# Optimization experiments

Measured on AMD Instinct MI355X. Metric: run time of the kernel, lower is better.

## Reference

```python
import jax, jax.numpy as jnp
import numpy as np

N_NODES = 20000
N_EDGES = 320000
IN_FEATS = 64
HIDDENS = [128, 128, 128]
K = 4        # n_kernels
DIM = 2      # pseudo_coord


def setup_inputs() -> dict:
    key = jax.random.key(0)
    ks = jax.random.split(key, 32)
    inp = {
        "features": jax.random.normal(ks[0], (N_NODES, IN_FEATS), dtype=jnp.float32),
        "pseudo": jax.random.uniform(ks[1], (N_EDGES, DIM), dtype=jnp.float32),
        "src": jax.random.randint(ks[2], (N_EDGES,), 0, N_NODES, dtype=jnp.int32),
        "dst": jax.random.randint(ks[3], (N_EDGES,), 0, N_NODES, dtype=jnp.int32),
    }
    dims_in = [IN_FEATS] + HIDDENS[:-1]
    ki = 4
    for i, (din, dout) in enumerate(zip(dims_in, HIDDENS)):
        inp[f"fc_w{i}"] = jax.random.normal(ks[ki], (din, K * dout), dtype=jnp.float32) * (1.0 / np.sqrt(din)); ki += 1
        inp[f"mu{i}"] = jax.random.normal(ks[ki], (K, DIM), dtype=jnp.float32) * 0.1; ki += 1
        inp[f"inv_sigma{i}"] = jnp.ones((K, DIM), dtype=jnp.float32)
        inp[f"bias{i}"] = jnp.zeros((dout,), dtype=jnp.float32)
        inp[f"pw{i}"] = jax.random.normal(ks[ki], (DIM, DIM), dtype=jnp.float32) * 0.5; ki += 1
        inp[f"pb{i}"] = jnp.zeros((DIM,), dtype=jnp.float32)
    return inp


def _gmm_layer(h, pseudo, src, dst, fc_w, mu, inv_sigma, bias, pw, pb):
    k, dim = mu.shape
    dout = fc_w.shape[1] // k
    hp = (h @ fc_w).reshape(-1, k, dout)              # [N, K, out]
    u = jnp.tanh(pseudo @ pw + pb)                    # [E, dim] per-layer pseudo projection
    diff = (u[:, None, :] - mu[None, :, :]) * inv_sigma[None, :, :]
    w = jnp.exp(-0.5 * jnp.sum(diff * diff, axis=-1))  # [E, K] Gaussian mixture weights
    msg = jnp.einsum('ek,eko->eo', w, hp[src])         # gather + weighted mix -> [E, out]
    agg = jax.ops.segment_sum(msg, dst, num_segments=h.shape[0])  # scatter-sum
    return agg + bias


def reference(features, pseudo, src, dst,
              fc_w0, mu0, inv_sigma0, bias0, pw0, pb0,
              fc_w1, mu1, inv_sigma1, bias1, pw1, pb1,
              fc_w2, mu2, inv_sigma2, bias2, pw2, pb2):
    h = features
    h = _gmm_layer(h, pseudo, src, dst, fc_w0, mu0, inv_sigma0, bias0, pw0, pb0)
    h = _gmm_layer(h, pseudo, src, dst, fc_w1, mu1, inv_sigma1, bias1, pw1, pb1)
    h = _gmm_layer(h, pseudo, src, dst, fc_w2, mu2, inv_sigma2, bias2, pw2, pb2)
    return h
```

## Files before the change

kernel.cpp:

```cpp
#include <hip/hip_runtime.h>
#include <hip/hip_bf16.h>
#include <hip/hip_fp16.h>
#include <math.h>

#define NN 20000
#define NE 320000

typedef __attribute__((ext_vector_type(8))) short bf16x8;
typedef __attribute__((ext_vector_type(4))) float f32x4;

__device__ inline float bf2f_lo(uint v) {
    union { uint i; float f; } c; c.i = v << 16; return c.f;
}
__device__ inline float bf2f_hi(uint v) {
    union { uint i; float f; } c; c.i = v & 0xffff0000u; return c.f;
}
__device__ inline ushort f2bf(float f) {
    __hip_bfloat16 h = __float2bfloat16(f);
    return *reinterpret_cast<ushort*>(&h);
}
__device__ inline float2 h2f2(uint u) {
    union { uint i; __half2 h; } c; c.i = u;
    return __half22float2(c.h);
}
__device__ inline ushort f2h(float f) {
    __half h = __float2half_rn(f);
    return *reinterpret_cast<ushort*>(&h);
}

__global__ void count_kernel(const int* __restrict__ dst, int* __restrict__ counts) {
    int e = blockIdx.x * blockDim.x + threadIdx.x;
    if (e < NE) atomicAdd(&counts[dst[e]], 1);
}

__global__ __launch_bounds__(1024) void scan_kernel(const int* __restrict__ counts,
                                                    int* __restrict__ offsets,
                                                    int* __restrict__ cursor) {
    __shared__ int part[1024];
    const int T = 1024, CHK = (NN + T - 1) / T;
    int t = threadIdx.x;
    int begin = t * CHK;
    int c[CHK];
    int s = 0;
    bool full = (begin + CHK <= NN);
    if (full) {
#pragma unroll
        for (int q = 0; q < CHK / 4; ++q) {
            int4 v = *(const int4*)(counts + begin + q * 4);
            c[q * 4 + 0] = v.x; c[q * 4 + 1] = v.y; c[q * 4 + 2] = v.z; c[q * 4 + 3] = v.w;
        }
#pragma unroll
        for (int q = 0; q < CHK; ++q) s += c[q];
    } else {
        int end = begin + CHK < NN ? begin + CHK : NN;
        if (begin > NN) begin = NN;
        for (int i = begin; i < end; ++i) {
            int v = counts[i];
            c[i - begin] = v;
            s += v;
        }
    }
    part[t] = s;
    __syncthreads();
    for (int off = 1; off < T; off <<= 1) {
        int v = (t >= off) ? part[t - off] : 0;
        __syncthreads();
        part[t] += v;
        __syncthreads();
    }
    int run = (t == 0) ? 0 : part[t - 1];
    if (full) {
#pragma unroll
        for (int q = 0; q < CHK / 4; ++q) {
            int4 o;
            o.x = run; run += c[q * 4 + 0];
            o.y = run; run += c[q * 4 + 1];
            o.z = run; run += c[q * 4 + 2];
            o.w = run; run += c[q * 4 + 3];
            *(int4*)(offsets + begin + q * 4) = o;
            *(int4*)(cursor + begin + q * 4) = o;
        }
    } else {
        int end = begin + CHK < NN ? begin + CHK : NN;
        for (int i = begin; i < end; ++i) {
            offsets[i] = run;
            cursor[i] = run;
            run += c[i - begin];
        }
    }
    if (t == T - 1) offsets[NN] = part[T - 1];
}

__global__ void fill1_kernel(const int* __restrict__ dst, int* __restrict__ cursor,
                             int* __restrict__ csr_eidx) {
    int e = blockIdx.x * blockDim.x + threadIdx.x;
    if (e >= NE) return;
    int pos = atomicAdd(&cursor[dst[e]], 1);
    csr_eidx[pos] = e;
}

struct EdgeParams {
    const float *pw0, *pb0, *mu0, *is0;
    const float *pw1, *pb1, *mu1, *is1;
    const float *pw2, *pb2, *mu2, *is2;
};

__device__ inline float fast_tanh(float x) {
    x = fminf(fmaxf(x, -9.f), 9.f);
    float e = __expf(2.f * x);
    return 1.f - 2.f / (e + 1.f);
}

__device__ inline void layer_w(float p0, float p1, const float* pw, const float* pb,
                               const float* mu, const float* is, float* out4) {
    float u0 = fast_tanh(p0 * pw[0] + p1 * pw[2] + pb[0]);
    float u1 = fast_tanh(p0 * pw[1] + p1 * pw[3] + pb[1]);
#pragma unroll
    for (int k = 0; k < 4; ++k) {
        float d0 = (u0 - mu[k * 2 + 0]) * is[k * 2 + 0];
        float d1 = (u1 - mu[k * 2 + 1]) * is[k * 2 + 1];
        out4[k] = __expf(-0.5f * (d0 * d0 + d1 * d1));
    }
}

__global__ void fill2_prep(const int* __restrict__ csr_eidx, const int* __restrict__ src,
                           const float* __restrict__ pseudo, EdgeParams P,
                           int* __restrict__ csr_src, ushort* __restrict__ csr_w,
                           const float* __restrict__ f0, const float* __restrict__ f1,
                           const float* __restrict__ f2, ushort* __restrict__ w0,
                           ushort* __restrict__ w1, ushort* __restrict__ w2) {
    int bid = blockIdx.x;
    if (bid < 1250) {
        int i = bid * 256 + threadIdx.x;
        int e = csr_eidx[i];
        float2 p = *(const float2*)(pseudo + (size_t)e * 2);
        csr_src[i] = src[e];
        float w[4];
        uint2 pk;
        layer_w(p.x, p.y, P.pw0, P.pb0, P.mu0, P.is0, w);
        pk.x = (uint)f2h(w[0]) | ((uint)f2h(w[1]) << 16);
        pk.y = (uint)f2h(w[2]) | ((uint)f2h(w[3]) << 16);
        *(uint2*)(csr_w + (size_t)(0 * NE + i) * 4) = pk;
        layer_w(p.x, p.y, P.pw1, P.pb1, P.mu1, P.is1, w);
        pk.x = (uint)f2h(w[0]) | ((uint)f2h(w[1]) << 16);
        pk.y = (uint)f2h(w[2]) | ((uint)f2h(w[3]) << 16);
        *(uint2*)(csr_w + (size_t)(1 * NE + i) * 4) = pk;
        layer_w(p.x, p.y, P.pw2, P.pb2, P.mu2, P.is2, w);
        pk.x = (uint)f2h(w[0]) | ((uint)f2h(w[1]) << 16);
        pk.y = (uint)f2h(w[2]) | ((uint)f2h(w[3]) << 16);
        *(uint2*)(csr_w + (size_t)(2 * NE + i) * 4) = pk;
    } else {
        int idx = (bid - 1250) * 256 + threadIdx.x;
        const float* srcp;
        ushort* dstp;
        int din, KD, li;
        if (idx < 128 * 256) {
            srcp = f0; dstp = w0; din = 64; KD = 256; li = idx;
        } else if (idx < 128 * 256 + 128 * 512) {
            srcp = f1; dstp = w1; din = 128; KD = 512; li = idx - 128 * 256;
        } else {
            srcp = f2; dstp = w2; din = 128; KD = 512; li = idx - 128 * 256 - 128 * 512;
        }
        int n = li / KD;
        int r = li - n * KD;
        int k = r / din;
        int d = r - k * din;
        dstp[li] = f2bf(srcp[d * 512 + k * 128 + n]);
    }
}

template <int DIN, bool INF32, bool OUTBF>
__global__ __launch_bounds__(256, 4) void layer_fused(const void* __restrict__ hin,
                                                      const int* __restrict__ offsets,
                                                      const int* __restrict__ csr_src,
                                                      const ushort* __restrict__ csr_w,
                                                      const ushort* __restrict__ Bt,
                                                      const float* __restrict__ bias,
                                                      void* __restrict__ hout) {
    constexpr int KD = 4 * DIN;
    constexpr int PITCH = KD + 8;
    constexpr int BATCH = 16;
    __shared__ __align__(16) ushort Ts[16 * PITCH];
    int wv = threadIdx.x >> 6, lane = threadIdx.x & 63;
    int l16 = lane & 15, quad = lane >> 4;
    int nb = blockIdx.x * 16;

#pragma unroll
    for (int j = 0; j < 4; ++j) {
        int row = wv * 4 + j;
        int n = nb + row;
        int b = __builtin_amdgcn_readfirstlane(offsets[n]);
        int e = __builtin_amdgcn_readfirstlane(offsets[n + 1]);
        if (INF32) {
            const float* h = (const float*)hin;
            float a0 = 0.f, a1 = 0.f, a2 = 0.f, a3 = 0.f;
            for (int i = b; i < e; i += BATCH) {
                int s[BATCH]; uint wlo[BATCH], whi[BATCH]; float hv[BATCH];
#pragma unroll
                for (int u = 0; u < BATCH; ++u) {
                    int ii = i + u;
                    bool ok = ii < e;
                    int idx = ok ? ii : b;
                    s[u] = csr_src[idx];
                    uint2 wp = *(const uint2*)(csr_w + (size_t)idx * 4);
                    wlo[u] = ok ? wp.x : 0u;
                    whi[u] = ok ? wp.y : 0u;
                }
#pragma unroll
                for (int u = 0; u < BATCH; ++u) hv[u] = h[(size_t)s[u] * 64 + lane];
#pragma unroll
                for (int u = 0; u < BATCH; ++u) {
                    float2 wa = h2f2(wlo[u]);
                    float2 wb = h2f2(whi[u]);
                    a0 += wa.x * hv[u];
                    a1 += wa.y * hv[u];
                    a2 += wb.x * hv[u];
                    a3 += wb.y * hv[u];
                }
            }
            Ts[row * PITCH + 0 * 64 + lane] = f2bf(a0);
            Ts[row * PITCH + 1 * 64 + lane] = f2bf(a1);
            Ts[row * PITCH + 2 * 64 + lane] = f2bf(a2);
            Ts[row * PITCH + 3 * 64 + lane] = f2bf(a3);
        } else {
            const ushort* h = (const ushort*)hin;
            float a00 = 0.f, a01 = 0.f, a10 = 0.f, a11 = 0.f;
            float a20 = 0.f, a21 = 0.f, a30 = 0.f, a31 = 0.f;
            for (int i = b; i < e; i += BATCH) {
                int s[BATCH]; uint wlo[BATCH], whi[BATCH]; uint v[BATCH];
#pragma unroll
                for (int u = 0; u < BATCH; ++u) {
                    int ii = i + u;
                    bool ok = ii < e;
                    int idx = ok ? ii : b;
                    s[u] = csr_src[idx];
                    uint2 wp = *(const uint2*)(csr_w + (size_t)idx * 4);
                    wlo[u] = ok ? wp.x : 0u;
                    whi[u] = ok ? wp.y : 0u;
                }
#pragma unroll
                for (int u = 0; u < BATCH; ++u)
                    v[u] = *(const uint*)(h + (size_t)s[u] * DIN + lane * 2);
#pragma unroll
                for (int u = 0; u < BATCH; ++u) {
                    float2 wa = h2f2(wlo[u]);
                    float2 wb = h2f2(whi[u]);
                    float lo = bf2f_lo(v[u]), hi = bf2f_hi(v[u]);
                    a00 += wa.x * lo; a01 += wa.x * hi;
                    a10 += wa.y * lo; a11 += wa.y * hi;
                    a20 += wb.x * lo; a21 += wb.x * hi;
                    a30 += wb.y * lo; a31 += wb.y * hi;
                }
            }
            ushort2 p;
            p.x = f2bf(a00); p.y = f2bf(a01);
            *(ushort2*)(Ts + row * PITCH + 0 * DIN + lane * 2) = p;
            p.x = f2bf(a10); p.y = f2bf(a11);
            *(ushort2*)(Ts + row * PITCH + 1 * DIN + lane * 2) = p;
            p.x = f2bf(a20); p.y = f2bf(a21);
            *(ushort2*)(Ts + row * PITCH + 2 * DIN + lane * 2) = p;
            p.x = f2bf(a30); p.y = f2bf(a31);
            *(ushort2*)(Ts + row * PITCH + 3 * DIN + lane * 2) = p;
        }
    }
    __syncthreads();

    f32x4 acc[2];
    acc[0] = (f32x4){0.f, 0.f, 0.f, 0.f};
    acc[1] = (f32x4){0.f, 0.f, 0.f, 0.f};
#pragma unroll 4
    for (int k0 = 0; k0 < KD; k0 += 32) {
        bf16x8 af = *(const bf16x8*)(Ts + l16 * PITCH + k0 + quad * 8);
#pragma unroll
        for (int c = 0; c < 2; ++c) {
            int nr = wv * 32 + c * 16 + l16;
            bf16x8 bfr = *(const bf16x8*)(Bt + (size_t)nr * KD + k0 + quad * 8);
            acc[c] = __builtin_amdgcn_mfma_f32_16x16x32_bf16(af, bfr, acc[c], 0, 0, 0);
        }
    }
#pragma unroll
    for (int c = 0; c < 2; ++c) {
        int gn = wv * 32 + c * 16 + l16;
        float bv = bias[gn];
#pragma unroll
        for (int i = 0; i < 4; ++i) {
            int gm = nb + quad * 4 + i;
            float val = acc[c][i] + bv;
            if (OUTBF)
                ((ushort*)hout)[(size_t)gm * 128 + gn] = f2bf(val);
            else
                ((float*)hout)[(size_t)gm * 128 + gn] = val;
        }
    }
}

extern "C" void kernel_launch(void* const* d_in, const int* in_sizes, int n_in,
                              void* d_out, int out_size, void* d_ws, size_t ws_size,
                              hipStream_t stream) {
    const float* features = (const float*)d_in[0];
    const float* pseudo = (const float*)d_in[1];
    const int* src = (const int*)d_in[2];
    const int* dst = (const int*)d_in[3];
    const float* fc_w[3] = {(const float*)d_in[4], (const float*)d_in[10], (const float*)d_in[16]};
    const float* mu[3] = {(const float*)d_in[5], (const float*)d_in[11], (const float*)d_in[17]};
    const float* isg[3] = {(const float*)d_in[6], (const float*)d_in[12], (const float*)d_in[18]};
    const float* bias[3] = {(const float*)d_in[7], (const float*)d_in[13], (const float*)d_in[19]};
    const float* pw[3] = {(const float*)d_in[8], (const float*)d_in[14], (const float*)d_in[20]};
    const float* pb[3] = {(const float*)d_in[9], (const float*)d_in[15], (const float*)d_in[21]};

    char* ws = (char*)d_ws;
    auto alloc = [&](size_t bytes) -> void* {
        void* p = (void*)ws;
        ws += (bytes + 255) & ~(size_t)255;
        return p;
    };
    int* counts = (int*)alloc((size_t)NN * 4);
    int* offsets = (int*)alloc((size_t)(NN + 1) * 4);
    int* cursor = (int*)alloc((size_t)NN * 4);
    int* csr_eidx = (int*)alloc((size_t)NE * 4);
    int* csr_src = (int*)alloc((size_t)NE * 4);
    ushort* csr_w = (ushort*)alloc((size_t)3 * NE * 4 * 2);
    ushort* w2t_0 = (ushort*)alloc((size_t)128 * 256 * 2);
    ushort* w2t_1 = (ushort*)alloc((size_t)128 * 512 * 2);
    ushort* w2t_2 = (ushort*)alloc((size_t)128 * 512 * 2);
    ushort* h1 = (ushort*)alloc((size_t)NN * 128 * 2);
    ushort* h2 = (ushort*)alloc((size_t)NN * 128 * 2);

    hipMemsetAsync(counts, 0, (size_t)NN * 4, stream);
    count_kernel<<<(NE + 255) / 256, 256, 0, stream>>>(dst, counts);
    scan_kernel<<<1, 1024, 0, stream>>>(counts, offsets, cursor);
    fill1_kernel<<<(NE + 255) / 256, 256, 0, stream>>>(dst, cursor, csr_eidx);

    EdgeParams P;
    P.pw0 = pw[0]; P.pb0 = pb[0]; P.mu0 = mu[0]; P.is0 = isg[0];
    P.pw1 = pw[1]; P.pb1 = pb[1]; P.mu1 = mu[1]; P.is1 = isg[1];
    P.pw2 = pw[2]; P.pb2 = pb[2]; P.mu2 = mu[2]; P.is2 = isg[2];
    fill2_prep<<<1890, 256, 0, stream>>>(csr_eidx, src, pseudo, P, csr_src, csr_w,
                                         fc_w[0], fc_w[1], fc_w[2], w2t_0, w2t_1, w2t_2);

    const int GB = NN / 16;

    layer_fused<64, true, true><<<GB, 256, 0, stream>>>(
        features, offsets, csr_src, csr_w + (size_t)0 * NE * 4, w2t_0, bias[0], h1);
    layer_fused<128, false, true><<<GB, 256, 0, stream>>>(
        h1, offsets, csr_src, csr_w + (size_t)1 * NE * 4, w2t_1, bias[1], h2);
    layer_fused<128, false, false><<<GB, 256, 0, stream>>>(
        h2, offsets, csr_src, csr_w + (size_t)2 * NE * 4, w2t_2, bias[2], (float*)d_out);
}
```

Baseline: 267.8 us.

## Split fused layer into aggregation and GEMM kernels; fuse CSR fill with edge weights

Each layer's fused aggregate+MFMA kernel becomes two kernels. The first aggregates one node per wave and writes the [N, K*Din] intermediate to a global buffer. The second is a separate 64-row-tile GEMM that reuses B fragments across four M sub-tiles. The CSR fill and the edge-weight computation are merged into one atomic-scatter kernel, which removes the csr_eidx indirection, and the weight transpose moves to its own kernel. This trades one extra global round trip of the intermediate per layer for better GEMM reuse and more parallelism in aggregation. Edge order within a node now depends on atomic order.

Result: slower. 292.5 us (+9.2%).

```diff
diff --git a/kernel.cpp b/kernel.cpp
--- a/kernel.cpp
+++ b/kernel.cpp
@@ -5,6 +5,7 @@
 
 #define NN 20000
 #define NE 320000
+#define NN_PAD 20032
 
 typedef __attribute__((ext_vector_type(8))) short bf16x8;
 typedef __attribute__((ext_vector_type(4))) float f32x4;
@@ -91,14 +92,6 @@
     if (t == T - 1) offsets[NN] = part[T - 1];
 }
 
-__global__ void fill1_kernel(const int* __restrict__ dst, int* __restrict__ cursor,
-                             int* __restrict__ csr_eidx) {
-    int e = blockIdx.x * blockDim.x + threadIdx.x;
-    if (e >= NE) return;
-    int pos = atomicAdd(&cursor[dst[e]], 1);
-    csr_eidx[pos] = e;
-}
-
 struct EdgeParams {
     const float *pw0, *pb0, *mu0, *is0;
     const float *pw1, *pb1, *mu1, *is1;
@@ -123,159 +116,165 @@
     }
 }
 
-__global__ void fill2_prep(const int* __restrict__ csr_eidx, const int* __restrict__ src,
-                           const float* __restrict__ pseudo, EdgeParams P,
-                           int* __restrict__ csr_src, ushort* __restrict__ csr_w,
-                           const float* __restrict__ f0, const float* __restrict__ f1,
-                           const float* __restrict__ f2, ushort* __restrict__ w0,
-                           ushort* __restrict__ w1, ushort* __restrict__ w2) {
-    int bid = blockIdx.x;
-    if (bid < 1250) {
-        int i = bid * 256 + threadIdx.x;
-        int e = csr_eidx[i];
-        float2 p = *(const float2*)(pseudo + (size_t)e * 2);
-        csr_src[i] = src[e];
-        float w[4];
-        uint2 pk;
-        layer_w(p.x, p.y, P.pw0, P.pb0, P.mu0, P.is0, w);
-        pk.x = (uint)f2h(w[0]) | ((uint)f2h(w[1]) << 16);
-        pk.y = (uint)f2h(w[2]) | ((uint)f2h(w[3]) << 16);
-        *(uint2*)(csr_w + (size_t)(0 * NE + i) * 4) = pk;
-        layer_w(p.x, p.y, P.pw1, P.pb1, P.mu1, P.is1, w);
-        pk.x = (uint)f2h(w[0]) | ((uint)f2h(w[1]) << 16);
-        pk.y = (uint)f2h(w[2]) | ((uint)f2h(w[3]) << 16);
-        *(uint2*)(csr_w + (size_t)(1 * NE + i) * 4) = pk;
-        layer_w(p.x, p.y, P.pw2, P.pb2, P.mu2, P.is2, w);
-        pk.x = (uint)f2h(w[0]) | ((uint)f2h(w[1]) << 16);
-        pk.y = (uint)f2h(w[2]) | ((uint)f2h(w[3]) << 16);
-        *(uint2*)(csr_w + (size_t)(2 * NE + i) * 4) = pk;
+__global__ void fill1_fused(const int* __restrict__ dst, const int* __restrict__ src,
+                            const float* __restrict__ pseudo, EdgeParams P,
+                            int* __restrict__ cursor, int* __restrict__ csr_src,
+                            ushort* __restrict__ csr_w) {
+    int e = blockIdx.x * blockDim.x + threadIdx.x;
+    if (e >= NE) return;
+    int pos = atomicAdd(&cursor[dst[e]], 1);
+    csr_src[pos] = src[e];
+    float2 p = *(const float2*)(pseudo + (size_t)e * 2);
+    float w[4];
+    uint2 pk;
+    layer_w(p.x, p.y, P.pw0, P.pb0, P.mu0, P.is0, w);
+    pk.x = (uint)f2h(w[0]) | ((uint)f2h(w[1]) << 16);
+    pk.y = (uint)f2h(w[2]) | ((uint)f2h(w[3]) << 16);
+    *(uint2*)(csr_w + (size_t)(0 * NE + pos) * 4) = pk;
+    layer_w(p.x, p.y, P.pw1, P.pb1, P.mu1, P.is1, w);
+    pk.x = (uint)f2h(w[0]) | ((uint)f2h(w[1]) << 16);
+    pk.y = (uint)f2h(w[2]) | ((uint)f2h(w[3]) << 16);
+    *(uint2*)(csr_w + (size_t)(1 * NE + pos) * 4) = pk;
+    layer_w(p.x, p.y, P.pw2, P.pb2, P.mu2, P.is2, w);
+    pk.x = (uint)f2h(w[0]) | ((uint)f2h(w[1]) << 16);
+    pk.y = (uint)f2h(w[2]) | ((uint)f2h(w[3]) << 16);
+    *(uint2*)(csr_w + (size_t)(2 * NE + pos) * 4) = pk;
+}
+
+__global__ void wtrans_kernel(const float* __restrict__ f0, const float* __restrict__ f1,
+                              const float* __restrict__ f2, ushort* __restrict__ w0,
+                              ushort* __restrict__ w1, ushort* __restrict__ w2) {
+    int idx = blockIdx.x * 256 + threadIdx.x;
+    const float* srcp;
+    ushort* dstp;
+    int din, KD, li;
+    if (idx < 128 * 256) {
+        srcp = f0; dstp = w0; din = 64; KD = 256; li = idx;
+    } else if (idx < 128 * 256 + 128 * 512) {
+        srcp = f1; dstp = w1; din = 128; KD = 512; li = idx - 128 * 256;
     } else {
-        int idx = (bid - 1250) * 256 + threadIdx.x;
-        const float* srcp;
-        ushort* dstp;
-        int din, KD, li;
-        if (idx < 128 * 256) {
-            srcp = f0; dstp = w0; din = 64; KD = 256; li = idx;
-        } else if (idx < 128 * 256 + 128 * 512) {
-            srcp = f1; dstp = w1; din = 128; KD = 512; li = idx - 128 * 256;
-        } else {
-            srcp = f2; dstp = w2; din = 128; KD = 512; li = idx - 128 * 256 - 128 * 512;
-        }
-        int n = li / KD;
-        int r = li - n * KD;
-        int k = r / din;
-        int d = r - k * din;
-        dstp[li] = f2bf(srcp[d * 512 + k * 128 + n]);
-    }
-}
-
-template <int DIN, bool INF32, bool OUTBF>
-__global__ __launch_bounds__(256, 4) void layer_fused(const void* __restrict__ hin,
-                                                      const int* __restrict__ offsets,
-                                                      const int* __restrict__ csr_src,
-                                                      const ushort* __restrict__ csr_w,
-                                                      const ushort* __restrict__ Bt,
-                                                      const float* __restrict__ bias,
-                                                      void* __restrict__ hout) {
+        srcp = f2; dstp = w2; din = 128; KD = 512; li = idx - 128 * 256 - 128 * 512;
+    }
+    int n = li / KD;
+    int r = li - n * KD;
+    int k = r / din;
+    int d = r - k * din;
+    dstp[li] = f2bf(srcp[d * 512 + k * 128 + n]);
+}
+
+template <int DIN, bool INF32>
+__global__ __launch_bounds__(256, 4) void agg_kernel(const void* __restrict__ hin,
+                                                     const int* __restrict__ offsets,
+                                                     const int* __restrict__ csr_src,
+                                                     const ushort* __restrict__ csr_w,
+                                                     ushort* __restrict__ T) {
     constexpr int KD = 4 * DIN;
-    constexpr int PITCH = KD + 8;
-    constexpr int BATCH = 16;
-    __shared__ __align__(16) ushort Ts[16 * PITCH];
+    constexpr int B = 8;
     int wv = threadIdx.x >> 6, lane = threadIdx.x & 63;
+    int n = blockIdx.x * 4 + wv;
+    int b = __builtin_amdgcn_readfirstlane(offsets[n]);
+    int e = __builtin_amdgcn_readfirstlane(offsets[n + 1]);
+    if (INF32) {
+        const float* h = (const float*)hin;
+        float a0 = 0.f, a1 = 0.f, a2 = 0.f, a3 = 0.f;
+        for (int i = b; i < e; i += B) {
+            int s[B]; uint wlo[B], whi[B]; float hv[B];
+#pragma unroll
+            for (int u = 0; u < B; ++u) {
+                int ii = i + u;
+                bool ok = ii < e;
+                int idx = ok ? ii : b;
+                s[u] = csr_src[idx];
+                uint2 wp = *(const uint2*)(csr_w + (size_t)idx * 4);
+                wlo[u] = ok ? wp.x : 0u;
+                whi[u] = ok ? wp.y : 0u;
+            }
+#pragma unroll
+            for (int u = 0; u < B; ++u) hv[u] = h[(size_t)s[u] * 64 + lane];
+#pragma unroll
+            for (int u = 0; u < B; ++u) {
+                float2 wa = h2f2(wlo[u]);
+                float2 wb = h2f2(whi[u]);
+                a0 += wa.x * hv[u];
+                a1 += wa.y * hv[u];
+                a2 += wb.x * hv[u];
+                a3 += wb.y * hv[u];
+            }
+        }
+        ushort* Tr = T + (size_t)n * KD;
+        Tr[0 * 64 + lane] = f2bf(a0);
+        Tr[1 * 64 + lane] = f2bf(a1);
+        Tr[2 * 64 + lane] = f2bf(a2);
+        Tr[3 * 64 + lane] = f2bf(a3);
+    } else {
+        const ushort* h = (const ushort*)hin;
+        float a00 = 0.f, a01 = 0.f, a10 = 0.f, a11 = 0.f;
+        float a20 = 0.f, a21 = 0.f, a30 = 0.f, a31 = 0.f;
+        for (int i = b; i < e; i += B) {
+            int s[B]; uint wlo[B], whi[B]; uint v[B];
+#pragma unroll
+            for (int u = 0; u < B; ++u) {
+                int ii = i + u;
+                bool ok = ii < e;
+                int idx = ok ? ii : b;
+                s[u] = csr_src[idx];
+                uint2 wp = *(const uint2*)(csr_w + (size_t)idx * 4);
+                wlo[u] = ok ? wp.x : 0u;
+                whi[u] = ok ? wp.y : 0u;
+            }
+#pragma unroll
+            for (int u = 0; u < B; ++u)
+                v[u] = *(const uint*)(h + (size_t)s[u] * DIN + lane * 2);
+#pragma unroll
+            for (int u = 0; u < B; ++u) {
+                float2 wa = h2f2(wlo[u]);
+                float2 wb = h2f2(whi[u]);
+                float lo = bf2f_lo(v[u]), hi = bf2f_hi(v[u]);
+                a00 += wa.x * lo; a01 += wa.x * hi;
+                a10 += wa.y * lo; a11 += wa.y * hi;
+                a20 += wb.x * lo; a21 += wb.x * hi;
+                a30 += wb.y * lo; a31 += wb.y * hi;
+            }
+        }
+        ushort* Tr = T + (size_t)n * KD;
+        ushort2 p;
+        p.x = f2bf(a00); p.y = f2bf(a01);
+        *(ushort2*)(Tr + 0 * DIN + lane * 2) = p;
+        p.x = f2bf(a10); p.y = f2bf(a11);
+        *(ushort2*)(Tr + 1 * DIN + lane * 2) = p;
+        p.x = f2bf(a20); p.y = f2bf(a21);
+        *(ushort2*)(Tr + 2 * DIN + lane * 2) = p;
+        p.x = f2bf(a30); p.y = f2bf(a31);
+        *(ushort2*)(Tr + 3 * DIN + lane * 2) = p;
+    }
+}
+
+template <int KD, bool OUTBF>
+__global__ __launch_bounds__(256) void gemm_kernel(const ushort* __restrict__ A,
+                                                   const ushort* __restrict__ Bt,
+                                                   const float* __restrict__ bias,
+                                                   void* __restrict__ out) {
+    int lane = threadIdx.x & 63, wv = threadIdx.x >> 6;
     int l16 = lane & 15, quad = lane >> 4;
-    int nb = blockIdx.x * 16;
-
-#pragma unroll
-    for (int j = 0; j < 4; ++j) {
-        int row = wv * 4 + j;
-        int n = nb + row;
-        int b = __builtin_amdgcn_readfirstlane(offsets[n]);
-        int e = __builtin_amdgcn_readfirstlane(offsets[n + 1]);
-        if (INF32) {
-            const float* h = (const float*)hin;
-            float a0 = 0.f, a1 = 0.f, a2 = 0.f, a3 = 0.f;
-            for (int i = b; i < e; i += BATCH) {
-                int s[BATCH]; uint wlo[BATCH], whi[BATCH]; float hv[BATCH];
-#pragma unroll
-                for (int u = 0; u < BATCH; ++u) {
-                    int ii = i + u;
-                    bool ok = ii < e;
-                    int idx = ok ? ii : b;
-                    s[u] = csr_src[idx];
-                    uint2 wp = *(const uint2*)(csr_w + (size_t)idx * 4);
-                    wlo[u] = ok ? wp.x : 0u;
-                    whi[u] = ok ? wp.y : 0u;
-                }
-#pragma unroll
-                for (int u = 0; u < BATCH; ++u) hv[u] = h[(size_t)s[u] * 64 + lane];
-#pragma unroll
-                for (int u = 0; u < BATCH; ++u) {
-                    float2 wa = h2f2(wlo[u]);
-                    float2 wb = h2f2(whi[u]);
-                    a0 += wa.x * hv[u];
-                    a1 += wa.y * hv[u];
-                    a2 += wb.x * hv[u];
-                    a3 += wb.y * hv[u];
-                }
-            }
-            Ts[row * PITCH + 0 * 64 + lane] = f2bf(a0);
-            Ts[row * PITCH + 1 * 64 + lane] = f2bf(a1);
-            Ts[row * PITCH + 2 * 64 + lane] = f2bf(a2);
-            Ts[row * PITCH + 3 * 64 + lane] = f2bf(a3);
-        } else {
-            const ushort* h = (const ushort*)hin;
-            float a00 = 0.f, a01 = 0.f, a10 = 0.f, a11 = 0.f;
-            float a20 = 0.f, a21 = 0.f, a30 = 0.f, a31 = 0.f;
-            for (int i = b; i < e; i += BATCH) {
-                int s[BATCH]; uint wlo[BATCH], whi[BATCH]; uint v[BATCH];
-#pragma unroll
-                for (int u = 0; u < BATCH; ++u) {
-                    int ii = i + u;
-                    bool ok = ii < e;
-                    int idx = ok ? ii : b;
-                    s[u] = csr_src[idx];
-                    uint2 wp = *(const uint2*)(csr_w + (size_t)idx * 4);
-                    wlo[u] = ok ? wp.x : 0u;
-                    whi[u] = ok ? wp.y : 0u;
-                }
-#pragma unroll
-                for (int u = 0; u < BATCH; ++u)
-                    v[u] = *(const uint*)(h + (size_t)s[u] * DIN + lane * 2);
-#pragma unroll
-                for (int u = 0; u < BATCH; ++u) {
-                    float2 wa = h2f2(wlo[u]);
-                    float2 wb = h2f2(whi[u]);
-                    float lo = bf2f_lo(v[u]), hi = bf2f_hi(v[u]);
-                    a00 += wa.x * lo; a01 += wa.x * hi;
-                    a10 += wa.y * lo; a11 += wa.y * hi;
-                    a20 += wb.x * lo; a21 += wb.x * hi;
-                    a30 += wb.y * lo; a31 += wb.y * hi;
-                }
-            }
-            ushort2 p;
-            p.x = f2bf(a00); p.y = f2bf(a01);
-            *(ushort2*)(Ts + row * PITCH + 0 * DIN + lane * 2) = p;
-            p.x = f2bf(a10); p.y = f2bf(a11);
-            *(ushort2*)(Ts + row * PITCH + 1 * DIN + lane * 2) = p;
-            p.x = f2bf(a20); p.y = f2bf(a21);
-            *(ushort2*)(Ts + row * PITCH + 2 * DIN + lane * 2) = p;
-            p.x = f2bf(a30); p.y = f2bf(a31);
-            *(ushort2*)(Ts + row * PITCH + 3 * DIN + lane * 2) = p;
-        }
-    }
-    __syncthreads();
-
-    f32x4 acc[2];
-    acc[0] = (f32x4){0.f, 0.f, 0.f, 0.f};
-    acc[1] = (f32x4){0.f, 0.f, 0.f, 0.f};
-#pragma unroll 4
+    int m0 = blockIdx.x * 64;
+    f32x4 acc[4][2];
+#pragma unroll
+    for (int mf = 0; mf < 4; ++mf)
+#pragma unroll
+        for (int c = 0; c < 2; ++c) acc[mf][c] = (f32x4){0.f, 0.f, 0.f, 0.f};
+#pragma unroll 2
     for (int k0 = 0; k0 < KD; k0 += 32) {
-        bf16x8 af = *(const bf16x8*)(Ts + l16 * PITCH + k0 + quad * 8);
+        bf16x8 bfr[2];
 #pragma unroll
         for (int c = 0; c < 2; ++c) {
             int nr = wv * 32 + c * 16 + l16;
-            bf16x8 bfr = *(const bf16x8*)(Bt + (size_t)nr * KD + k0 + quad * 8);
-            acc[c] = __builtin_amdgcn_mfma_f32_16x16x32_bf16(af, bfr, acc[c], 0, 0, 0);
+            bfr[c] = *(const bf16x8*)(Bt + (size_t)nr * KD + k0 + quad * 8);
+        }
+#pragma unroll
+        for (int mf = 0; mf < 4; ++mf) {
+            bf16x8 af = *(const bf16x8*)(A + (size_t)(m0 + mf * 16 + l16) * KD + k0 + quad * 8);
+            acc[mf][0] = __builtin_amdgcn_mfma_f32_16x16x32_bf16(af, bfr[0], acc[mf][0], 0, 0, 0);
+            acc[mf][1] = __builtin_amdgcn_mfma_f32_16x16x32_bf16(af, bfr[1], acc[mf][1], 0, 0, 0);
         }
     }
 #pragma unroll
@@ -283,13 +282,18 @@
         int gn = wv * 32 + c * 16 + l16;
         float bv = bias[gn];
 #pragma unroll
-        for (int i = 0; i < 4; ++i) {
-            int gm = nb + quad * 4 + i;
-            float val = acc[c][i] + bv;
-            if (OUTBF)
-                ((ushort*)hout)[(size_t)gm * 128 + gn] = f2bf(val);
-            else
-                ((float*)hout)[(size_t)gm * 128 + gn] = val;
+        for (int mf = 0; mf < 4; ++mf) {
+#pragma unroll
+            for (int i = 0; i < 4; ++i) {
+                int gm = m0 + mf * 16 + quad * 4 + i;
+                if (gm < NN) {
+                    float val = acc[mf][c][i] + bv;
+                    if (OUTBF)
+                        ((ushort*)out)[(size_t)gm * 128 + gn] = f2bf(val);
+                    else
+                        ((float*)out)[(size_t)gm * 128 + gn] = val;
+                }
+            }
         }
     }
 }
@@ -317,33 +321,36 @@
     int* counts = (int*)alloc((size_t)NN * 4);
     int* offsets = (int*)alloc((size_t)(NN + 1) * 4);
     int* cursor = (int*)alloc((size_t)NN * 4);
-    int* csr_eidx = (int*)alloc((size_t)NE * 4);
     int* csr_src = (int*)alloc((size_t)NE * 4);
     ushort* csr_w = (ushort*)alloc((size_t)3 * NE * 4 * 2);
     ushort* w2t_0 = (ushort*)alloc((size_t)128 * 256 * 2);
     ushort* w2t_1 = (ushort*)alloc((size_t)128 * 512 * 2);
     ushort* w2t_2 = (ushort*)alloc((size_t)128 * 512 * 2);
+    ushort* Tbuf = (ushort*)alloc((size_t)NN_PAD * 512 * 2);
     ushort* h1 = (ushort*)alloc((size_t)NN * 128 * 2);
     ushort* h2 = (ushort*)alloc((size_t)NN * 128 * 2);
 
     hipMemsetAsync(counts, 0, (size_t)NN * 4, stream);
     count_kernel<<<(NE + 255) / 256, 256, 0, stream>>>(dst, counts);
+    wtrans_kernel<<<640, 256, 0, stream>>>(fc_w[0], fc_w[1], fc_w[2], w2t_0, w2t_1, w2t_2);
     scan_kernel<<<1, 1024, 0, stream>>>(counts, offsets, cursor);
-    fill1_kernel<<<(NE + 255) / 256, 256, 0, stream>>>(dst, cursor, csr_eidx);
 
     EdgeParams P;
     P.pw0 = pw[0]; P.pb0 = pb[0]; P.mu0 = mu[0]; P.is0 = isg[0];
     P.pw1 = pw[1]; P.pb1 = pb[1]; P.mu1 = mu[1]; P.is1 = isg[1];
     P.pw2 = pw[2]; P.pb2 = pb[2]; P.mu2 = mu[2]; P.is2 = isg[2];
-    fill2_prep<<<1890, 256, 0, stream>>>(csr_eidx, src, pseudo, P, csr_src, csr_w,
-                                         fc_w[0], fc_w[1], fc_w[2], w2t_0, w2t_1, w2t_2);
-
-    const int GB = NN / 16;
-
-    layer_fused<64, true, true><<<GB, 256, 0, stream>>>(
-        features, offsets, csr_src, csr_w + (size_t)0 * NE * 4, w2t_0, bias[0], h1);
-    layer_fused<128, false, true><<<GB, 256, 0, stream>>>(
-        h1, offsets, csr_src, csr_w + (size_t)1 * NE * 4, w2t_1, bias[1], h2);
-    layer_fused<128, false, false><<<GB, 256, 0, stream>>>(
-        h2, offsets, csr_src, csr_w + (size_t)2 * NE * 4, w2t_2, bias[2], (float*)d_out);
-}
+    fill1_fused<<<(NE + 255) / 256, 256, 0, stream>>>(dst, src, pseudo, P, cursor, csr_src, csr_w);
+
+    const int GA = NN / 4;
+    const int GG = NN_PAD / 64;
+
+    agg_kernel<64, true><<<GA, 256, 0, stream>>>(features, offsets, csr_src,
+                                                 csr_w + (size_t)0 * NE * 4, Tbuf);
+    gemm_kernel<256, true><<<GG, 256, 0, stream>>>(Tbuf, w2t_0, bias[0], h1);
+    agg_kernel<128, false><<<GA, 256, 0, stream>>>(h1, offsets, csr_src,
+                                                   csr_w + (size_t)1 * NE * 4, Tbuf);
+    gemm_kernel<512, true><<<GG, 256, 0, stream>>>(Tbuf, w2t_1, bias[1], h2);
+    agg_kernel<128, false><<<GA, 256, 0, stream>>>(h2, offsets, csr_src,
+                                                   csr_w + (size_t)2 * NE * 4, Tbuf);
+    gemm_kernel<512, false><<<GG, 256, 0, stream>>>(Tbuf, w2t_2, bias[2], (float*)d_out);
+}
```
